# Kernel optimization log

Hardware: AMD Instinct MI355X
Metric: run time of the kernel (lower is better)

The kernel has to match this reference:

```python
import jax, jax.numpy as jnp
import numpy as np

N_NODES = 100000
N_EDGES = 1600000
NUM_GRAPHS = 1024
D_IN = 128
D_HID = 128
D_OUT = 2
LN_EPS = 1e-5


def setup_inputs() -> dict:
    key = jax.random.key(0)
    ks = jax.random.split(key, 10)
    x = jax.random.normal(ks[0], (N_NODES, D_IN), dtype=jnp.float32)
    edge_index = jax.random.randint(ks[1], (2, N_EDGES), 0, N_NODES, dtype=jnp.int64)
    batch = jnp.sort(jax.random.randint(ks[2], (N_NODES,), 0, NUM_GRAPHS, dtype=jnp.int64))
    s = 0.05  # weight scale to keep activations sane
    return {
        "x": x,
        "edge_index": edge_index,
        "batch": batch,
        "W1l": jax.random.normal(ks[3], (D_HID, D_IN), dtype=jnp.float32) * s,
        "b1l": jnp.zeros((D_HID,), dtype=jnp.float32),
        "W1r": jax.random.normal(ks[4], (D_HID, D_IN), dtype=jnp.float32) * s,
        "W2l": jax.random.normal(ks[5], (D_HID, D_HID), dtype=jnp.float32) * s,
        "b2l": jnp.zeros((D_HID,), dtype=jnp.float32),
        "W2r": jax.random.normal(ks[6], (D_HID, D_HID), dtype=jnp.float32) * s,
        "ln_g": jnp.ones((D_HID,), dtype=jnp.float32),
        "ln_b": jnp.zeros((D_HID,), dtype=jnp.float32),
        "Wlin": jax.random.normal(ks[7], (D_OUT, D_HID), dtype=jnp.float32) * s,
        "blin": jnp.zeros((D_OUT,), dtype=jnp.float32),
    }


def _sage_conv(x, src, dst, Wl, bl, Wr):
    # PyG SAGEConv with mean aggregation: lin_l(mean_{j in N(i)} x_j) + lin_r(x_i)
    msg_sum = jax.ops.segment_sum(x[src], dst, num_segments=N_NODES)
    deg = jax.ops.segment_sum(jnp.ones((src.shape[0], 1), x.dtype), dst, num_segments=N_NODES)
    agg = msg_sum / jnp.maximum(deg, 1.0)  # isolated nodes -> 0
    return agg @ Wl.T + bl + x @ Wr.T  # lin_r has no bias (PyG default)


def reference(x, edge_index, batch, W1l, b1l, W1r, W2l, b2l, W2r, ln_g, ln_b, Wlin, blin):
    src, dst = edge_index[0], edge_index[1]
    h = jax.nn.relu(_sage_conv(x, src, dst, W1l, b1l, W1r))
    h = jax.nn.relu(_sage_conv(h, src, dst, W2l, b2l, W2r))
    # global_add_pool over graphs
    g = jax.ops.segment_sum(h, batch, num_segments=NUM_GRAPHS)  # [G, D_HID]
    # LayerNorm over last dim
    mu = jnp.mean(g, axis=-1, keepdims=True)
    var = jnp.var(g, axis=-1, keepdims=True)
    gn = (g - mu) * jax.lax.rsqrt(var + LN_EPS) * ln_g + ln_b
    return gn @ Wlin.T + blin  # [G, D_OUT]
```

## Files before the change

### kernel.cpp

```cpp
#include <hip/hip_runtime.h>
#include <hip/hip_bf16.h>

#define N_NODES   100000
#define N_EDGES   1600000
#define NUM_GRAPHS 1024
#define D         128
#define LN_EPS    1e-5f
#define NBUCKETS  196
#define CAP       9216
#define CHUNK     4096

typedef __attribute__((ext_vector_type(8))) short short8;
typedef __attribute__((ext_vector_type(4))) float floatx4;
typedef __attribute__((ext_vector_type(2))) float f32x2;

static __device__ __forceinline__ float bf2f(unsigned int u) {
    return __uint_as_float(u << 16);
}
static __device__ __forceinline__ unsigned short f2bf(float f) {
    __hip_bfloat16 h = __float2bfloat16(f);
    return *reinterpret_cast<unsigned short*>(&h);
}
static __device__ __forceinline__ void acc4(f32x2* acc, uint4 v) {
    acc[0] += (f32x2){__uint_as_float(v.x << 16), __uint_as_float(v.x & 0xffff0000u)};
    acc[1] += (f32x2){__uint_as_float(v.y << 16), __uint_as_float(v.y & 0xffff0000u)};
    acc[2] += (f32x2){__uint_as_float(v.z << 16), __uint_as_float(v.z & 0xffff0000u)};
    acc[3] += (f32x2){__uint_as_float(v.w << 16), __uint_as_float(v.w & 0xffff0000u)};
}

__global__ __launch_bounds__(256)
void prep_kernel(const float* __restrict__ x, unsigned short* __restrict__ xbf,
                 const float* __restrict__ W1l, const float* __restrict__ W1r,
                 const float* __restrict__ W2l, const float* __restrict__ W2r,
                 unsigned short* __restrict__ Wc1, unsigned short* __restrict__ Wc2,
                 int* __restrict__ cursor) {
    int i = blockIdx.x * 256 + threadIdx.x;
    float4 v = reinterpret_cast<const float4*>(x)[i];
    ushort4 o;
    o.x = f2bf(v.x); o.y = f2bf(v.y); o.z = f2bf(v.z); o.w = f2bf(v.w);
    reinterpret_cast<ushort4*>(xbf)[i] = o;
    if (blockIdx.x < 256) {
        int layer = i >> 15;
        int rem = i & 32767;
        int c = rem >> 8;
        int k = rem & 255;
        const float* Wl = layer ? W2l : W1l;
        const float* Wr = layer ? W2r : W1r;
        unsigned short* dst = layer ? Wc2 : Wc1;
        float wv = (k < 128) ? Wl[c * 128 + k] : Wr[c * 128 + (k - 128)];
        dst[c * 256 + k] = f2bf(wv);
    }
    if (blockIdx.x == 256 && threadIdx.x < NBUCKETS)
        cursor[threadIdx.x] = threadIdx.x * CAP;
}

__global__ __launch_bounds__(256)
void bin_scatter_kernel(const int* __restrict__ src, const int* __restrict__ dst,
                        int* __restrict__ cursor, uint2* __restrict__ binned) {
    __shared__ int cnt[NBUCKETS];
    __shared__ int base[NBUCKETS];
    int chunkBase = blockIdx.x * CHUNK;
    for (int i = threadIdx.x; i < NBUCKETS; i += 256) cnt[i] = 0;
    __syncthreads();
    int es[16], ed[16], lofs[16];
    #pragma unroll
    for (int j = 0; j < 16; ++j) {
        int e = chunkBase + j * 256 + threadIdx.x;
        if (e < N_EDGES) {
            es[j] = src[e];
            ed[j] = dst[e];
            lofs[j] = atomicAdd(&cnt[ed[j] >> 9], 1);
        }
    }
    __syncthreads();
    for (int i = threadIdx.x; i < NBUCKETS; i += 256) {
        int c = cnt[i];
        base[i] = c ? atomicAdd(&cursor[i], c) : 0;
    }
    __syncthreads();
    #pragma unroll
    for (int j = 0; j < 16; ++j) {
        int e = chunkBase + j * 256 + threadIdx.x;
        if (e < N_EDGES) {
            int b = ed[j] >> 9;
            int pos = base[b] + lofs[j];
            if (pos < (b + 1) * CAP)
                binned[pos] = make_uint2((unsigned)es[j], (unsigned)ed[j]);
        }
    }
}

__global__ __launch_bounds__(512)
void bucket_build_kernel(const uint2* __restrict__ binned, const int* __restrict__ cursor,
                         int2* __restrict__ row_info, int* __restrict__ src_sorted) {
    __shared__ int scnt[512];
    __shared__ int sscan[512];
    int b = blockIdx.x;
    int t = threadIdx.x;
    int lo = b * CAP;
    int hi = cursor[b];
    scnt[t] = 0;
    __syncthreads();
    for (int e = lo + t; e < hi; e += 512)
        atomicAdd(&scnt[binned[e].y & 511], 1);
    __syncthreads();
    int v = scnt[t];
    sscan[t] = v;
    __syncthreads();
    for (int off = 1; off < 512; off <<= 1) {
        int a = (t >= off) ? sscan[t - off] : 0;
        __syncthreads();
        sscan[t] += a;
        __syncthreads();
    }
    int ex = sscan[t] - v;
    int node = b * 512 + t;
    if (node < N_NODES) row_info[node] = make_int2(lo + ex, v);
    scnt[t] = ex;
    __syncthreads();
    for (int e = lo + t; e < hi; e += 512) {
        uint2 r = binned[e];
        int p = atomicAdd(&scnt[r.y & 511], 1);
        src_sorted[lo + p] = (int)r.x;
    }
}

__global__ __launch_bounds__(256)
void aggregate_kernel(const unsigned short* __restrict__ feat,
                      const int* __restrict__ src_sorted,
                      const int2* __restrict__ row_info,
                      unsigned short* __restrict__ aggout) {
    int wave = threadIdx.x >> 6;
    int lane = threadIdx.x & 63;
    int node = blockIdx.x * 4 + wave;
    int sub = lane >> 4;
    int ch = (lane & 15) * 8;
    int2 ri = row_info[node];
    int s = ri.x, deg = ri.y;
    const unsigned short* fb = feat + ch;
    f32x2 acc[4];
    acc[0] = acc[1] = acc[2] = acc[3] = (f32x2){0.f, 0.f};

    if (deg <= 64) {
        int si = 0;
        if (lane < deg) si = src_sorted[s + lane];
        int rounds = (deg + 3) >> 2;
        for (int r = 0; r < rounds; ++r) {
            int eidx = r * 4 + sub;
            int u = __shfl(si, eidx, 64);
            if (eidx < deg) {
                uint4 v = *(const uint4*)(fb + (size_t)u * 128);
                acc4(acc, v);
            }
        }
    } else {
        for (int j = s + sub; j < s + deg; j += 4) {
            int u = src_sorted[j];
            uint4 v = *(const uint4*)(fb + (size_t)u * 128);
            acc4(acc, v);
        }
    }
    #pragma unroll
    for (int i = 0; i < 4; ++i) {
        acc[i].x += __shfl_xor(acc[i].x, 16, 64);
        acc[i].y += __shfl_xor(acc[i].y, 16, 64);
        acc[i].x += __shfl_xor(acc[i].x, 32, 64);
        acc[i].y += __shfl_xor(acc[i].y, 32, 64);
    }
    float inv = 1.f / (float)(deg > 1 ? deg : 1);
    if (sub == 0) {
        uint4 ov;
        ov.x = (unsigned)f2bf(acc[0].x * inv) | ((unsigned)f2bf(acc[0].y * inv) << 16);
        ov.y = (unsigned)f2bf(acc[1].x * inv) | ((unsigned)f2bf(acc[1].y * inv) << 16);
        ov.z = (unsigned)f2bf(acc[2].x * inv) | ((unsigned)f2bf(acc[2].y * inv) << 16);
        ov.w = (unsigned)f2bf(acc[3].x * inv) | ((unsigned)f2bf(acc[3].y * inv) << 16);
        *(uint4*)(aggout + (size_t)node * 128 + ch) = ov;
    }
}

__global__ __launch_bounds__(256)
void gemm_kernel(const unsigned short* __restrict__ A1,
                 const unsigned short* __restrict__ A2,
                 const unsigned short* __restrict__ Wcat,
                 const float* __restrict__ bias,
                 unsigned short* __restrict__ out) {
    __shared__ unsigned short Asm[64][32];
    __shared__ unsigned short Wsm[128][32];
    int tid = threadIdx.x;
    int wave = tid >> 6;
    int lane = tid & 63;
    int nodeBase = blockIdx.x * 64;
    floatx4 acc[4][2];
    #pragma unroll
    for (int a = 0; a < 4; ++a)
        #pragma unroll
        for (int b = 0; b < 2; ++b) acc[a][b] = (floatx4){0.f, 0.f, 0.f, 0.f};

    int r = tid >> 2, sg = tid & 3;
    int quad = lane >> 4, m = lane & 15;

    for (int kc = 0; kc < 8; ++kc) {
        const unsigned short* Asrc = (kc < 4) ? A1 : A2;
        int kOff = (kc & 3) * 32;
        int node = nodeBase + r;
        float4 av = make_float4(0.f, 0.f, 0.f, 0.f);
        if (node < N_NODES) av = *(const float4*)(Asrc + (size_t)node * 128 + kOff + sg * 8);
        *(float4*)(&Asm[r][sg * 8]) = av;
        #pragma unroll
        for (int it = 0; it < 2; ++it) {
            int idx = tid + it * 256;
            int wr = idx >> 2, wsg = idx & 3;
            *(float4*)(&Wsm[wr][wsg * 8]) = *(const float4*)(Wcat + wr * 256 + kc * 32 + wsg * 8);
        }
        __syncthreads();
        short8 afr[4], bfr[2];
        #pragma unroll
        for (int nb = 0; nb < 4; ++nb)
            afr[nb] = *(const short8*)(&Asm[nb * 16 + m][quad * 8]);
        #pragma unroll
        for (int cb = 0; cb < 2; ++cb)
            bfr[cb] = *(const short8*)(&Wsm[wave * 32 + cb * 16 + m][quad * 8]);
        #pragma unroll
        for (int nb = 0; nb < 4; ++nb)
            #pragma unroll
            for (int cb = 0; cb < 2; ++cb)
                acc[nb][cb] = __builtin_amdgcn_mfma_f32_16x16x32_bf16(afr[nb], bfr[cb], acc[nb][cb], 0, 0, 0);
        __syncthreads();
    }
    #pragma unroll
    for (int cb = 0; cb < 2; ++cb) {
        int col = wave * 32 + cb * 16 + m;
        float bv = bias[col];
        #pragma unroll
        for (int nb = 0; nb < 4; ++nb) {
            #pragma unroll
            for (int rr = 0; rr < 4; ++rr) {
                int row = nodeBase + nb * 16 + quad * 4 + rr;
                if (row < N_NODES) {
                    float v = acc[nb][cb][rr] + bv;
                    v = v > 0.f ? v : 0.f;
                    out[(size_t)row * 128 + col] = f2bf(v);
                }
            }
        }
    }
}

__global__ __launch_bounds__(256)
void pool_ln_out_kernel(const unsigned short* __restrict__ h2,
                        const int* __restrict__ batch,
                        const float* __restrict__ ln_g, const float* __restrict__ ln_b,
                        const float* __restrict__ Wlin, const float* __restrict__ blin,
                        float* __restrict__ out) {
    int g = blockIdx.x;
    int t = threadIdx.x;
    int lane = t & 63, w = t >> 6;
    __shared__ int se[2];
    if (t < 2) {
        int target = g + t;
        int lo = 0, hi = N_NODES;
        while (lo < hi) {
            int mid = (lo + hi) >> 1;
            if (batch[mid] < target) lo = mid + 1; else hi = mid;
        }
        se[t] = lo;
    }
    __syncthreads();
    int s = se[0], e = se[1];
    int ns = t >> 4;
    int chg = t & 15;
    f32x2 a[4];
    a[0] = a[1] = a[2] = a[3] = (f32x2){0.f, 0.f};
    for (int n = s + ns; n < e; n += 16) {
        uint4 v = *(const uint4*)(h2 + (size_t)n * 128 + chg * 8);
        acc4(a, v);
    }
    #pragma unroll
    for (int i = 0; i < 4; ++i) {
        a[i].x += __shfl_xor(a[i].x, 16, 64);
        a[i].y += __shfl_xor(a[i].y, 16, 64);
        a[i].x += __shfl_xor(a[i].x, 32, 64);
        a[i].y += __shfl_xor(a[i].y, 32, 64);
    }
    __shared__ float sw[4][128];
    if (lane < 16) {
        #pragma unroll
        for (int k = 0; k < 4; ++k) {
            sw[w][chg * 8 + 2 * k]     = a[k].x;
            sw[w][chg * 8 + 2 * k + 1] = a[k].y;
        }
    }
    __syncthreads();
    __shared__ float red[128];
    float sum = 0.f;
    if (t < 128) {
        sum = sw[0][t] + sw[1][t] + sw[2][t] + sw[3][t];
        red[t] = sum;
    }
    __syncthreads();
    for (int off = 64; off > 0; off >>= 1) {
        if (t < off) red[t] += red[t + off];
        __syncthreads();
    }
    float mu = red[0] * (1.f / 128.f);
    __syncthreads();
    float dv = sum - mu;
    if (t < 128) red[t] = dv * dv;
    __syncthreads();
    for (int off = 64; off > 0; off >>= 1) {
        if (t < off) red[t] += red[t + off];
        __syncthreads();
    }
    float var = red[0] * (1.f / 128.f);
    __syncthreads();
    __shared__ float r0[128], r1[128];
    if (t < 128) {
        float gn = dv * rsqrtf(var + LN_EPS) * ln_g[t] + ln_b[t];
        r0[t] = gn * Wlin[t];
        r1[t] = gn * Wlin[128 + t];
    }
    __syncthreads();
    for (int off = 64; off > 0; off >>= 1) {
        if (t < off) { r0[t] += r0[t + off]; r1[t] += r1[t + off]; }
        __syncthreads();
    }
    if (t == 0) {
        out[g * 2 + 0] = r0[0] + blin[0];
        out[g * 2 + 1] = r1[0] + blin[1];
    }
}

extern "C" void kernel_launch(void* const* d_in, const int* in_sizes, int n_in,
                              void* d_out, int out_size, void* d_ws, size_t ws_size,
                              hipStream_t stream) {
    const float* x    = (const float*)d_in[0];
    const int*   ei   = (const int*)d_in[1];
    const int*   batch= (const int*)d_in[2];
    const float* W1l  = (const float*)d_in[3];
    const float* b1l  = (const float*)d_in[4];
    const float* W1r  = (const float*)d_in[5];
    const float* W2l  = (const float*)d_in[6];
    const float* b2l  = (const float*)d_in[7];
    const float* W2r  = (const float*)d_in[8];
    const float* ln_g = (const float*)d_in[9];
    const float* ln_b = (const float*)d_in[10];
    const float* Wlin = (const float*)d_in[11];
    const float* blin = (const float*)d_in[12];
    float* out = (float*)d_out;

    char* ws = (char*)d_ws;
    size_t off = 0;
    auto alloc = [&](size_t bytes) {
        char* p = ws + off;
        off = (off + bytes + 255) & ~(size_t)255;
        return p;
    };
    unsigned short* xbf  = (unsigned short*)alloc((size_t)N_NODES * D * 2);
    unsigned short* aggb = (unsigned short*)alloc((size_t)N_NODES * D * 2);
    unsigned short* h1   = (unsigned short*)alloc((size_t)N_NODES * D * 2);
    unsigned short* Wc1  = (unsigned short*)alloc(128 * 256 * 2);
    unsigned short* Wc2  = (unsigned short*)alloc(128 * 256 * 2);
    int2* row_info   = (int2*)alloc((size_t)N_NODES * 8);
    int* src_sorted  = (int*)alloc((size_t)NBUCKETS * CAP * 4);
    int* cursor      = (int*)alloc(NBUCKETS * 4);
    uint2* binned = (uint2*)aggb;

    const int* srcI = ei;
    const int* dstI = ei + N_EDGES;

    prep_kernel<<<12500, 256, 0, stream>>>(x, xbf, W1l, W1r, W2l, W2r, Wc1, Wc2, cursor);
    bin_scatter_kernel<<<(N_EDGES + CHUNK - 1) / CHUNK, 256, 0, stream>>>(srcI, dstI, cursor, binned);
    bucket_build_kernel<<<NBUCKETS, 512, 0, stream>>>(binned, cursor, row_info, src_sorted);

    aggregate_kernel<<<25000, 256, 0, stream>>>(xbf, src_sorted, row_info, aggb);
    gemm_kernel<<<1563, 256, 0, stream>>>(aggb, xbf, Wc1, b1l, h1);
    aggregate_kernel<<<25000, 256, 0, stream>>>(h1, src_sorted, row_info, aggb);
    gemm_kernel<<<1563, 256, 0, stream>>>(aggb, h1, Wc2, b2l, xbf);
    pool_ln_out_kernel<<<NUM_GRAPHS, 256, 0, stream>>>(xbf, batch, ln_g, ln_b, Wlin, blin, out);
}
```

Measured before the change: 329.3 us.

## Fuse mean aggregation with SAGE GEMM into one per-layer kernel

Merges the neighbor-gather aggregation and the dual-weight GEMM into one kernel per layer. Each block aggregates 64 nodes into padded shared memory and reads the root-feature half of the A operand straight from global memory. This drops the intermediate aggregate buffer's write and reread and two launches. In exchange it cuts the number of waves doing gathers, since each wave now handles 16 nodes serially instead of one node per wave across 25000 blocks. It also drops the shuffle-based low-degree path, which may reduce latency hiding in the memory-bound gather.

```diff
diff --git a/kernel.cpp b/kernel.cpp
--- a/kernel.cpp
+++ b/kernel.cpp
@@ -9,6 +9,7 @@
 #define NBUCKETS  196
 #define CAP       9216
 #define CHUNK     4096
+#define APAD      136
 
 typedef __attribute__((ext_vector_type(8))) short short8;
 typedef __attribute__((ext_vector_type(4))) float floatx4;
@@ -126,86 +127,64 @@
 }
 
 __global__ __launch_bounds__(256)
-void aggregate_kernel(const unsigned short* __restrict__ feat,
-                      const int* __restrict__ src_sorted,
-                      const int2* __restrict__ row_info,
-                      unsigned short* __restrict__ aggout) {
-    int wave = threadIdx.x >> 6;
-    int lane = threadIdx.x & 63;
-    int node = blockIdx.x * 4 + wave;
+void fused_layer_kernel(const unsigned short* __restrict__ feat,
+                        const int* __restrict__ src_sorted,
+                        const int2* __restrict__ row_info,
+                        const unsigned short* __restrict__ Wcat,
+                        const float* __restrict__ bias,
+                        unsigned short* __restrict__ out) {
+    __shared__ unsigned short Asm[64][APAD];
+    __shared__ unsigned short Wsm[128][32];
+    int tid = threadIdx.x;
+    int wave = tid >> 6;
+    int lane = tid & 63;
     int sub = lane >> 4;
     int ch = (lane & 15) * 8;
-    int2 ri = row_info[node];
-    int s = ri.x, deg = ri.y;
+    int nodeBase = blockIdx.x * 64;
     const unsigned short* fb = feat + ch;
-    f32x2 acc[4];
-    acc[0] = acc[1] = acc[2] = acc[3] = (f32x2){0.f, 0.f};
-
-    if (deg <= 64) {
-        int si = 0;
-        if (lane < deg) si = src_sorted[s + lane];
-        int rounds = (deg + 3) >> 2;
-        for (int r = 0; r < rounds; ++r) {
-            int eidx = r * 4 + sub;
-            int u = __shfl(si, eidx, 64);
-            if (eidx < deg) {
-                uint4 v = *(const uint4*)(fb + (size_t)u * 128);
-                acc4(acc, v);
-            }
-        }
-    } else {
+
+    for (int i = 0; i < 16; ++i) {
+        int nl = wave * 16 + i;
+        int node = nodeBase + nl;
+        int s = 0, deg = 0;
+        if (node < N_NODES) {
+            int2 ri = row_info[node];
+            s = ri.x; deg = ri.y;
+        }
+        f32x2 acc[4];
+        acc[0] = acc[1] = acc[2] = acc[3] = (f32x2){0.f, 0.f};
         for (int j = s + sub; j < s + deg; j += 4) {
             int u = src_sorted[j];
             uint4 v = *(const uint4*)(fb + (size_t)u * 128);
             acc4(acc, v);
         }
-    }
-    #pragma unroll
-    for (int i = 0; i < 4; ++i) {
-        acc[i].x += __shfl_xor(acc[i].x, 16, 64);
-        acc[i].y += __shfl_xor(acc[i].y, 16, 64);
-        acc[i].x += __shfl_xor(acc[i].x, 32, 64);
-        acc[i].y += __shfl_xor(acc[i].y, 32, 64);
-    }
-    float inv = 1.f / (float)(deg > 1 ? deg : 1);
-    if (sub == 0) {
-        uint4 ov;
-        ov.x = (unsigned)f2bf(acc[0].x * inv) | ((unsigned)f2bf(acc[0].y * inv) << 16);
-        ov.y = (unsigned)f2bf(acc[1].x * inv) | ((unsigned)f2bf(acc[1].y * inv) << 16);
-        ov.z = (unsigned)f2bf(acc[2].x * inv) | ((unsigned)f2bf(acc[2].y * inv) << 16);
-        ov.w = (unsigned)f2bf(acc[3].x * inv) | ((unsigned)f2bf(acc[3].y * inv) << 16);
-        *(uint4*)(aggout + (size_t)node * 128 + ch) = ov;
-    }
-}
-
-__global__ __launch_bounds__(256)
-void gemm_kernel(const unsigned short* __restrict__ A1,
-                 const unsigned short* __restrict__ A2,
-                 const unsigned short* __restrict__ Wcat,
-                 const float* __restrict__ bias,
-                 unsigned short* __restrict__ out) {
-    __shared__ unsigned short Asm[64][32];
-    __shared__ unsigned short Wsm[128][32];
-    int tid = threadIdx.x;
-    int wave = tid >> 6;
-    int lane = tid & 63;
-    int nodeBase = blockIdx.x * 64;
+        #pragma unroll
+        for (int k = 0; k < 4; ++k) {
+            acc[k].x += __shfl_xor(acc[k].x, 16, 64);
+            acc[k].y += __shfl_xor(acc[k].y, 16, 64);
+            acc[k].x += __shfl_xor(acc[k].x, 32, 64);
+            acc[k].y += __shfl_xor(acc[k].y, 32, 64);
+        }
+        float inv = 1.f / (float)(deg > 1 ? deg : 1);
+        if (sub == 0) {
+            uint4 ov;
+            ov.x = (unsigned)f2bf(acc[0].x * inv) | ((unsigned)f2bf(acc[0].y * inv) << 16);
+            ov.y = (unsigned)f2bf(acc[1].x * inv) | ((unsigned)f2bf(acc[1].y * inv) << 16);
+            ov.z = (unsigned)f2bf(acc[2].x * inv) | ((unsigned)f2bf(acc[2].y * inv) << 16);
+            ov.w = (unsigned)f2bf(acc[3].x * inv) | ((unsigned)f2bf(acc[3].y * inv) << 16);
+            *(uint4*)(&Asm[nl][ch]) = ov;
+        }
+    }
+    __syncthreads();
+
+    int quad = lane >> 4, m = lane & 15;
     floatx4 acc[4][2];
     #pragma unroll
     for (int a = 0; a < 4; ++a)
         #pragma unroll
         for (int b = 0; b < 2; ++b) acc[a][b] = (floatx4){0.f, 0.f, 0.f, 0.f};
 
-    int r = tid >> 2, sg = tid & 3;
-    int quad = lane >> 4, m = lane & 15;
-
     for (int kc = 0; kc < 8; ++kc) {
-        const unsigned short* Asrc = (kc < 4) ? A1 : A2;
-        int kOff = (kc & 3) * 32;
-        int node = nodeBase + r;
-        float4 av = make_float4(0.f, 0.f, 0.f, 0.f);
-        if (node < N_NODES) av = *(const float4*)(Asrc + (size_t)node * 128 + kOff + sg * 8);
-        *(float4*)(&Asm[r][sg * 8]) = av;
         #pragma unroll
         for (int it = 0; it < 2; ++it) {
             int idx = tid + it * 256;
@@ -214,9 +193,21 @@
         }
         __syncthreads();
         short8 afr[4], bfr[2];
-        #pragma unroll
-        for (int nb = 0; nb < 4; ++nb)
-            afr[nb] = *(const short8*)(&Asm[nb * 16 + m][quad * 8]);
+        if (kc < 4) {
+            #pragma unroll
+            for (int nb = 0; nb < 4; ++nb)
+                afr[nb] = *(const short8*)(&Asm[nb * 16 + m][kc * 32 + quad * 8]);
+        } else {
+            int kOff = (kc - 4) * 32 + quad * 8;
+            #pragma unroll
+            for (int nb = 0; nb < 4; ++nb) {
+                int row = nodeBase + nb * 16 + m;
+                if (row < N_NODES)
+                    afr[nb] = *(const short8*)(feat + (size_t)row * 128 + kOff);
+                else
+                    afr[nb] = (short8){0,0,0,0,0,0,0,0};
+            }
+        }
         #pragma unroll
         for (int cb = 0; cb < 2; ++cb)
             bfr[cb] = *(const short8*)(&Wsm[wave * 32 + cb * 16 + m][quad * 8]);
@@ -356,14 +347,13 @@
         return p;
     };
     unsigned short* xbf  = (unsigned short*)alloc((size_t)N_NODES * D * 2);
-    unsigned short* aggb = (unsigned short*)alloc((size_t)N_NODES * D * 2);
     unsigned short* h1   = (unsigned short*)alloc((size_t)N_NODES * D * 2);
     unsigned short* Wc1  = (unsigned short*)alloc(128 * 256 * 2);
     unsigned short* Wc2  = (unsigned short*)alloc(128 * 256 * 2);
     int2* row_info   = (int2*)alloc((size_t)N_NODES * 8);
     int* src_sorted  = (int*)alloc((size_t)NBUCKETS * CAP * 4);
     int* cursor      = (int*)alloc(NBUCKETS * 4);
-    uint2* binned = (uint2*)aggb;
+    uint2* binned    = (uint2*)alloc((size_t)NBUCKETS * CAP * 8);
 
     const int* srcI = ei;
     const int* dstI = ei + N_EDGES;
@@ -372,9 +362,7 @@
     bin_scatter_kernel<<<(N_EDGES + CHUNK - 1) / CHUNK, 256, 0, stream>>>(srcI, dstI, cursor, binned);
     bucket_build_kernel<<<NBUCKETS, 512, 0, stream>>>(binned, cursor, row_info, src_sorted);
 
-    aggregate_kernel<<<25000, 256, 0, stream>>>(xbf, src_sorted, row_info, aggb);
-    gemm_kernel<<<1563, 256, 0, stream>>>(aggb, xbf, Wc1, b1l, h1);
-    aggregate_kernel<<<25000, 256, 0, stream>>>(h1, src_sorted, row_info, aggb);
-    gemm_kernel<<<1563, 256, 0, stream>>>(aggb, h1, Wc2, b2l, xbf);
+    fused_layer_kernel<<<1563, 256, 0, stream>>>(xbf, src_sorted, row_info, Wc1, b1l, h1);
+    fused_layer_kernel<<<1563, 256, 0, stream>>>(h1, src_sorted, row_info, Wc2, b2l, xbf);
     pool_ln_out_kernel<<<NUM_GRAPHS, 256, 0, stream>>>(xbf, batch, ln_g, ln_b, Wlin, blin, out);
 }
```

After: 448.2 us. 36.1% more time.

## Pack binned edges into 32-bit records and use smaller 256-node buckets

Applied to the files above, without the earlier changes.

Doubles the bucket count so each bucket covers 256 destination nodes, and packs each binned edge as a single 32-bit word holding the 17-bit source plus the local destination index. The bucket build keeps the records and their atomic ranks in registers, so it reads the binned array once instead of twice. This halves the binned traffic and gives the CSR build twice as many blocks for parallelism. The cost is a fixed register budget of 19 records per thread, which caps bucket size at CAP, and packing that assumes node ids fit in 17 bits.

```diff
diff --git a/kernel.cpp b/kernel.cpp
--- a/kernel.cpp
+++ b/kernel.cpp
@@ -6,8 +6,8 @@
 #define NUM_GRAPHS 1024
 #define D         128
 #define LN_EPS    1e-5f
-#define NBUCKETS  196
-#define CAP       9216
+#define NBUCKETS  391
+#define CAP       4864
 #define CHUNK     4096
 
 typedef __attribute__((ext_vector_type(8))) short short8;
@@ -50,13 +50,15 @@
         float wv = (k < 128) ? Wl[c * 128 + k] : Wr[c * 128 + (k - 128)];
         dst[c * 256 + k] = f2bf(wv);
     }
-    if (blockIdx.x == 256 && threadIdx.x < NBUCKETS)
-        cursor[threadIdx.x] = threadIdx.x * CAP;
+    if (blockIdx.x == 256) {
+        for (int b = threadIdx.x; b < NBUCKETS; b += 256)
+            cursor[b] = b * CAP;
+    }
 }
 
 __global__ __launch_bounds__(256)
 void bin_scatter_kernel(const int* __restrict__ src, const int* __restrict__ dst,
-                        int* __restrict__ cursor, uint2* __restrict__ binned) {
+                        int* __restrict__ cursor, unsigned* __restrict__ binned) {
     __shared__ int cnt[NBUCKETS];
     __shared__ int base[NBUCKETS];
     int chunkBase = blockIdx.x * CHUNK;
@@ -69,7 +71,7 @@
         if (e < N_EDGES) {
             es[j] = src[e];
             ed[j] = dst[e];
-            lofs[j] = atomicAdd(&cnt[ed[j] >> 9], 1);
+            lofs[j] = atomicAdd(&cnt[ed[j] >> 8], 1);
         }
     }
     __syncthreads();
@@ -82,46 +84,60 @@
     for (int j = 0; j < 16; ++j) {
         int e = chunkBase + j * 256 + threadIdx.x;
         if (e < N_EDGES) {
-            int b = ed[j] >> 9;
+            int b = ed[j] >> 8;
             int pos = base[b] + lofs[j];
             if (pos < (b + 1) * CAP)
-                binned[pos] = make_uint2((unsigned)es[j], (unsigned)ed[j]);
-        }
-    }
-}
-
-__global__ __launch_bounds__(512)
-void bucket_build_kernel(const uint2* __restrict__ binned, const int* __restrict__ cursor,
+                binned[pos] = ((unsigned)(ed[j] & 255) << 17) | (unsigned)es[j];
+        }
+    }
+}
+
+__global__ __launch_bounds__(256)
+void bucket_build_kernel(const unsigned* __restrict__ binned, const int* __restrict__ cursor,
                          int2* __restrict__ row_info, int* __restrict__ src_sorted) {
-    __shared__ int scnt[512];
-    __shared__ int sscan[512];
+    __shared__ int scnt[256];
+    __shared__ int sscan[256];
     int b = blockIdx.x;
     int t = threadIdx.x;
     int lo = b * CAP;
     int hi = cursor[b];
+    int cap_end = lo + CAP;
+    if (hi > cap_end) hi = cap_end;
     scnt[t] = 0;
     __syncthreads();
-    for (int e = lo + t; e < hi; e += 512)
-        atomicAdd(&scnt[binned[e].y & 511], 1);
+    unsigned rec[19];
+    short rnk[19];
+    #pragma unroll
+    for (int i = 0; i < 19; ++i) {
+        int e = lo + t + i * 256;
+        if (e < hi) {
+            unsigned r = binned[e];
+            rec[i] = r;
+            rnk[i] = (short)atomicAdd(&scnt[r >> 17], 1);
+        }
+    }
     __syncthreads();
     int v = scnt[t];
     sscan[t] = v;
     __syncthreads();
-    for (int off = 1; off < 512; off <<= 1) {
+    for (int off = 1; off < 256; off <<= 1) {
         int a = (t >= off) ? sscan[t - off] : 0;
         __syncthreads();
         sscan[t] += a;
         __syncthreads();
     }
     int ex = sscan[t] - v;
-    int node = b * 512 + t;
+    int node = b * 256 + t;
     if (node < N_NODES) row_info[node] = make_int2(lo + ex, v);
     scnt[t] = ex;
     __syncthreads();
-    for (int e = lo + t; e < hi; e += 512) {
-        uint2 r = binned[e];
-        int p = atomicAdd(&scnt[r.y & 511], 1);
-        src_sorted[lo + p] = (int)r.x;
+    #pragma unroll
+    for (int i = 0; i < 19; ++i) {
+        int e = lo + t + i * 256;
+        if (e < hi) {
+            unsigned r = rec[i];
+            src_sorted[lo + scnt[r >> 17] + rnk[i]] = (int)(r & 0x1FFFFu);
+        }
     }
 }
 
@@ -363,14 +379,14 @@
     int2* row_info   = (int2*)alloc((size_t)N_NODES * 8);
     int* src_sorted  = (int*)alloc((size_t)NBUCKETS * CAP * 4);
     int* cursor      = (int*)alloc(NBUCKETS * 4);
-    uint2* binned = (uint2*)aggb;
+    unsigned* binned = (unsigned*)aggb;
 
     const int* srcI = ei;
     const int* dstI = ei + N_EDGES;
 
     prep_kernel<<<12500, 256, 0, stream>>>(x, xbf, W1l, W1r, W2l, W2r, Wc1, Wc2, cursor);
     bin_scatter_kernel<<<(N_EDGES + CHUNK - 1) / CHUNK, 256, 0, stream>>>(srcI, dstI, cursor, binned);
-    bucket_build_kernel<<<NBUCKETS, 512, 0, stream>>>(binned, cursor, row_info, src_sorted);
+    bucket_build_kernel<<<NBUCKETS, 256, 0, stream>>>(binned, cursor, row_info, src_sorted);
 
     aggregate_kernel<<<25000, 256, 0, stream>>>(xbf, src_sorted, row_info, aggb);
     gemm_kernel<<<1563, 256, 0, stream>>>(aggb, xbf, Wc1, b1l, h1);
```

Measured after the change: 329.5 us. No clear change (+0.1%).
